# Kernel tuning notes

Measured on AMD Instinct MI355X. Metric: run time of the kernel, lower is better.

## Reference

```python
import jax, jax.numpy as jnp
import numpy as np

N, B, E, H = 131072, 4096, 512, 8
D = E // H

def setup_inputs() -> dict:
    key = jax.random.key(0)
    ks = jax.random.split(key, 20)
    def lin_w(k, fan_out, fan_in):
        return (jax.random.normal(k, (fan_out, fan_in), dtype=jnp.float32)
                * (1.0 / np.sqrt(fan_in)).astype(np.float32))
    node_features = jax.random.normal(ks[0], (N, E), dtype=jnp.float32)
    # segment ids sorted, guaranteed to cover every graph 0..B-1
    extra = jax.random.randint(ks[1], (N - B,), 0, B)
    batch = jnp.sort(jnp.concatenate([jnp.arange(B), extra])).astype(jnp.int32)
    scaffold_embedding = jax.random.normal(ks[2], (B, E), dtype=jnp.float32)
    return {
        'node_features': node_features,
        'scaffold_embedding': scaffold_embedding,
        'Wq': lin_w(ks[3], E, E), 'bq': jnp.zeros((E,), jnp.float32),
        'Wk': lin_w(ks[4], E, E), 'bk': jnp.zeros((E,), jnp.float32),
        'Wv': lin_w(ks[5], E, E), 'bv': jnp.zeros((E,), jnp.float32),
        'in_proj_w': lin_w(ks[6], 3 * E, E),
        'in_proj_b': jnp.zeros((3 * E,), jnp.float32),
        'mha_out_w': lin_w(ks[7], E, E), 'mha_out_b': jnp.zeros((E,), jnp.float32),
        'out_w': lin_w(ks[8], E, E), 'out_b': jnp.zeros((E,), jnp.float32),
        'ln_g': jnp.ones((E,), jnp.float32), 'ln_b': jnp.zeros((E,), jnp.float32),
        'batch': batch,
    }

def reference(node_features, scaffold_embedding, Wq, bq, Wk, bk, Wv, bv,
              in_proj_w, in_proj_b, mha_out_w, mha_out_b,
              out_w, out_b, ln_g, ln_b, batch):
    Bsz = scaffold_embedding.shape[0]
    # module's own q/k/v projections
    q = scaffold_embedding @ Wq.T + bq            # [B, E]
    k = node_features @ Wk.T + bk                 # [N, E]
    v = node_features @ Wv.T + bv                 # [N, E]
    # nn.MultiheadAttention internal in-projection
    Wiq, Wik, Wiv = jnp.split(in_proj_w, 3, axis=0)
    biq, bik, biv = jnp.split(in_proj_b, 3, axis=0)
    qq = (q @ Wiq.T + biq).reshape(Bsz, H, D)     # [B, H, D]
    kk = (k @ Wik.T + bik).reshape(-1, H, D)      # [N, H, D]
    vv = (v @ Wiv.T + biv).reshape(-1, H, D)      # [N, H, D]
    # per-node logit against its graph's single query (segment attention)
    scale = 1.0 / np.sqrt(D).astype(np.float32)
    logits = jnp.einsum('nhd,nhd->nh', kk, qq[batch]) * scale  # [N, H]
    m = jax.ops.segment_max(logits, batch, num_segments=B)     # [B, H]
    p = jnp.exp(logits - m[batch])
    Z = jax.ops.segment_sum(p, batch, num_segments=B)          # [B, H]
    w = p / Z[batch]                                           # [N, H]
    pooled = jax.ops.segment_sum(w[:, :, None] * vv, batch,
                                 num_segments=B).reshape(Bsz, E)
    # MHA out-projection, then module out_proj, dropout (eval=identity), LayerNorm
    out = pooled @ mha_out_w.T + mha_out_b
    out = out @ out_w.T + out_b
    mu = out.mean(axis=-1, keepdims=True)
    var = out.var(axis=-1, keepdims=True)
    return (out - mu) / jnp.sqrt(var + 1e-5) * ln_g + ln_b
```

## Files before the change

kernel.cpp:

```cpp
#include <hip/hip_runtime.h>
#include <hip/hip_bf16.h>
#include <cstdint>
#include <type_traits>

typedef __attribute__((ext_vector_type(8))) short short8v;
typedef __attribute__((ext_vector_type(8))) unsigned short ushort8v;
typedef __attribute__((ext_vector_type(4))) float f32x4;

__device__ __forceinline__ unsigned short f2bf(float f) {
    unsigned u = __builtin_bit_cast(unsigned, f);
    u = (u + 0x7fffu + ((u >> 16) & 1u)) >> 16;
    return (unsigned short)u;
}
__device__ __forceinline__ float bf2f(unsigned short s) {
    return __builtin_bit_cast(float, ((unsigned)s) << 16);
}
__device__ __forceinline__ unsigned cvtpk(float lo, float hi) {
    unsigned r;
    asm("v_cvt_pk_bf16_f32 %0, %1, %2" : "=v"(r) : "v"(lo), "v"(hi));
    return r;
}

template <typename TA, typename TW, bool C_BF16>
__device__ __forceinline__ void gemm_core(
    const TA* __restrict__ A, int lda,
    const TW* __restrict__ W, int ldw,
    void* __restrict__ Cp, int ldc,
    const float* __restrict__ bias, int K, size_t cbase,
    int bx, int by, unsigned short* As, unsigned short* Bs)
{
    const int tid  = threadIdx.x;
    const int lane = tid & 63;
    const int wave = tid >> 6;
    const int wr = wave >> 1, wc = wave & 1;
    const size_t row0 = (size_t)by * 128;
    const size_t col0 = (size_t)bx * 128;
    const int nk = K >> 6;

    f32x4 acc[4][4];
#pragma unroll
    for (int i = 0; i < 4; ++i)
#pragma unroll
        for (int j = 0; j < 4; ++j) acc[i][j] = f32x4{0.f, 0.f, 0.f, 0.f};

    float saf[4][8]; ushort8v sab[4];
    float swf[4][8]; ushort8v swb[4];

    auto load_tile = [&](int kt) {
#pragma unroll
        for (int it = 0; it < 4; ++it) {
            int g = tid + it * 256;
            int r = g >> 3, c8 = g & 7;
            if constexpr (std::is_same<TA, float>::value) {
                const float4* ap = reinterpret_cast<const float4*>(A + (row0 + r) * (size_t)lda + kt * 64 + c8 * 8);
                float4 a0 = ap[0], a1 = ap[1];
                saf[it][0] = a0.x; saf[it][1] = a0.y; saf[it][2] = a0.z; saf[it][3] = a0.w;
                saf[it][4] = a1.x; saf[it][5] = a1.y; saf[it][6] = a1.z; saf[it][7] = a1.w;
            } else {
                sab[it] = *reinterpret_cast<const ushort8v*>(A + (row0 + r) * (size_t)lda + kt * 64 + c8 * 8);
            }
            if constexpr (std::is_same<TW, float>::value) {
                const float4* wp = reinterpret_cast<const float4*>(W + (col0 + r) * (size_t)ldw + kt * 64 + c8 * 8);
                float4 w0 = wp[0], w1 = wp[1];
                swf[it][0] = w0.x; swf[it][1] = w0.y; swf[it][2] = w0.z; swf[it][3] = w0.w;
                swf[it][4] = w1.x; swf[it][5] = w1.y; swf[it][6] = w1.z; swf[it][7] = w1.w;
            } else {
                swb[it] = *reinterpret_cast<const ushort8v*>(W + (col0 + r) * (size_t)ldw + kt * 64 + c8 * 8);
            }
        }
    };
    auto write_tile = [&]() {
#pragma unroll
        for (int it = 0; it < 4; ++it) {
            int g = tid + it * 256;
            int r = g >> 3, c8 = g & 7;
            int idx = r * 64 + ((c8 ^ (r & 7)) << 3);
            if constexpr (std::is_same<TA, float>::value) {
                uint4 av;
                av.x = cvtpk(saf[it][0], saf[it][1]); av.y = cvtpk(saf[it][2], saf[it][3]);
                av.z = cvtpk(saf[it][4], saf[it][5]); av.w = cvtpk(saf[it][6], saf[it][7]);
                *reinterpret_cast<uint4*>(&As[idx]) = av;
            } else {
                *reinterpret_cast<ushort8v*>(&As[idx]) = sab[it];
            }
            if constexpr (std::is_same<TW, float>::value) {
                uint4 wv;
                wv.x = cvtpk(swf[it][0], swf[it][1]); wv.y = cvtpk(swf[it][2], swf[it][3]);
                wv.z = cvtpk(swf[it][4], swf[it][5]); wv.w = cvtpk(swf[it][6], swf[it][7]);
                *reinterpret_cast<uint4*>(&Bs[idx]) = wv;
            } else {
                *reinterpret_cast<ushort8v*>(&Bs[idx]) = swb[it];
            }
        }
    };

    load_tile(0);
    for (int kt = 0; kt < nk; ++kt) {
        __syncthreads();
        write_tile();
        __syncthreads();
        if (kt + 1 < nk) load_tile(kt + 1);
#pragma unroll
        for (int kk = 0; kk < 2; ++kk) {
            short8v af[4], bfv[4];
#pragma unroll
            for (int mi = 0; mi < 4; ++mi) {
                int r = wr * 64 + mi * 16 + (lane & 15);
                int slot = kk * 4 + (lane >> 4);
                af[mi] = *reinterpret_cast<const short8v*>(&As[r * 64 + ((slot ^ (r & 7)) << 3)]);
            }
#pragma unroll
            for (int ni = 0; ni < 4; ++ni) {
                int r = wc * 64 + ni * 16 + (lane & 15);
                int slot = kk * 4 + (lane >> 4);
                bfv[ni] = *reinterpret_cast<const short8v*>(&Bs[r * 64 + ((slot ^ (r & 7)) << 3)]);
            }
#pragma unroll
            for (int mi = 0; mi < 4; ++mi)
#pragma unroll
                for (int ni = 0; ni < 4; ++ni)
                    acc[mi][ni] = __builtin_amdgcn_mfma_f32_16x16x32_bf16(af[mi], bfv[ni], acc[mi][ni], 0, 0, 0);
        }
    }

#pragma unroll
    for (int ni = 0; ni < 4; ++ni) {
        size_t col = col0 + wc * 64 + ni * 16 + (lane & 15);
        float bv = bias ? bias[col] : 0.0f;
#pragma unroll
        for (int mi = 0; mi < 4; ++mi) {
#pragma unroll
            for (int q = 0; q < 4; ++q) {
                size_t row = row0 + wr * 64 + mi * 16 + ((lane >> 4) << 2) + q;
                float v = acc[mi][ni][q] + bv;
                if constexpr (C_BF16)
                    ((unsigned short*)Cp)[cbase + row * (size_t)ldc + col] = f2bf(v);
                else
                    ((float*)Cp)[cbase + row * (size_t)ldc + col] = v;
            }
        }
    }
}

template <typename TA, typename TW, bool C_BF16>
__global__ __launch_bounds__(256) void gemm_awt(
    const TA* __restrict__ A, int lda, const TW* __restrict__ W, int ldw,
    void* __restrict__ Cp, int ldc, const float* __restrict__ bias, int K,
    int az, int wz, size_t cz)
{
    __shared__ __attribute__((aligned(16))) unsigned short As[128 * 64];
    __shared__ __attribute__((aligned(16))) unsigned short Bs[128 * 64];
    gemm_core<TA, TW, C_BF16>(A + (size_t)blockIdx.z * az, lda,
                              W + (size_t)blockIdx.z * wz, ldw,
                              Cp, ldc, bias, K, (size_t)blockIdx.z * cz,
                              blockIdx.x, blockIdx.y, As, Bs);
}

struct WG4 { const float* A[4]; const float* W[4]; unsigned short* C[4]; };
__global__ __launch_bounds__(256) void gemm_w4(WG4 a)
{
    __shared__ __attribute__((aligned(16))) unsigned short As[128 * 64];
    __shared__ __attribute__((aligned(16))) unsigned short Bs[128 * 64];
    int z = blockIdx.z;
    gemm_core<float, float, true>(a.A[z], 512, a.W[z], 512, a.C[z], 512,
                                  nullptr, 512, 0, blockIdx.x, blockIdx.y, As, Bs);
}

__global__ void transpose4_512(const float* __restrict__ s0, float* __restrict__ d0,
                               const float* __restrict__ s1, float* __restrict__ d1,
                               const float* __restrict__ s2, float* __restrict__ d2,
                               const float* __restrict__ s3, float* __restrict__ d3)
{
    const float* src; float* dst;
    switch (blockIdx.z) {
        case 0: src = s0; dst = d0; break;
        case 1: src = s1; dst = d1; break;
        case 2: src = s2; dst = d2; break;
        default: src = s3; dst = d3; break;
    }
    __shared__ float t[32][33];
    int tx = threadIdx.x, ty = threadIdx.y;
    int bx = blockIdx.x * 32, by = blockIdx.y * 32;
#pragma unroll
    for (int j = 0; j < 4; ++j) t[ty + j * 8][tx] = src[(size_t)(by + ty + j * 8) * 512 + bx + tx];
    __syncthreads();
#pragma unroll
    for (int j = 0; j < 4; ++j) dst[(size_t)(bx + ty + j * 8) * 512 + by + tx] = t[tx][ty + j * 8];
}

struct BiasArgs { const float* W[3]; const float* vin[3]; const float* vadd[3]; float* out[3]; };
__global__ void bias_combine3(BiasArgs a)
{
    int which = blockIdx.y, e = blockIdx.x, lane = threadIdx.x;
    const float* W = a.W[which] + (size_t)e * 512 + lane * 8;
    const float* v = a.vin[which] + lane * 8;
    float s = 0.f;
#pragma unroll
    for (int j = 0; j < 8; ++j) s += W[j] * v[j];
#pragma unroll
    for (int st = 1; st < 64; st <<= 1) s += __shfl_xor(s, st, 64);
    if (lane == 0) a.out[which][e] = s + a.vadd[which][e];
}
__global__ void bias_combine_bf(const unsigned short* __restrict__ W, const float* __restrict__ vin,
                                const float* __restrict__ vadd, float* __restrict__ out)
{
    int e = blockIdx.x, lane = threadIdx.x;
    ushort8v wv = *reinterpret_cast<const ushort8v*>(W + (size_t)e * 512 + lane * 8);
    const float* v = vin + lane * 8;
    float s = 0.f;
#pragma unroll
    for (int j = 0; j < 8; ++j) s += bf2f(wv[j]) * v[j];
#pragma unroll
    for (int st = 1; st < 64; st <<= 1) s += __shfl_xor(s, st, 64);
    if (lane == 0) out[e] = s + vadd[e];
}

#define CHUNK 32
__global__ __launch_bounds__(256) void attn_pool(
    const float* __restrict__ X, const unsigned short* __restrict__ G,
    const int* __restrict__ batch, unsigned short* __restrict__ xw, int Nn)
{
    __shared__ __attribute__((aligned(16))) unsigned short Xs[CHUNK * 512];
    __shared__ __attribute__((aligned(16))) unsigned short Gs[8 * 512];
    __shared__ float lg[CHUNK * 8];
    __shared__ float red[256];
    __shared__ float mh[8], Zh[8], sch[8];

    const int b = blockIdx.x, t = threadIdx.x;
    const int lane = t & 63, wvx = t >> 6;

    int lo = 0, hi = Nn;
    while (lo < hi) { int mid = (lo + hi) >> 1; if (batch[mid] < b) lo = mid + 1; else hi = mid; }
    const int s = lo;
    hi = Nn;
    while (lo < hi) { int mid = (lo + hi) >> 1; if (batch[mid] < b + 1) lo = mid + 1; else hi = mid; }
    const int e = lo;

    if (t < 8) { mh[t] = -1e30f; Zh[t] = 0.f; }
    {
        const uint4* gp = reinterpret_cast<const uint4*>(G + (size_t)b * 4096);
        reinterpret_cast<uint4*>(Gs)[t] = gp[t];
        reinterpret_cast<uint4*>(Gs)[t + 256] = gp[t + 256];
    }

    float acc[16];
#pragma unroll
    for (int i = 0; i < 16; ++i) acc[i] = 0.f;

    for (int base = s; base < e; base += CHUNK) {
        const int cnt = min(CHUNK, e - base);
        __syncthreads();
#pragma unroll
        for (int i = 0; i < 8; ++i) {
            int u = t + 256 * i;
            int j = u >> 6;
            int col = (u & 63) * 8;
            uint4 w;
            if (j < cnt) {
                const float4* ap = reinterpret_cast<const float4*>(X + (size_t)(base + j) * 512 + col);
                float4 a0 = ap[0], a1 = ap[1];
                w.x = cvtpk(a0.x, a0.y); w.y = cvtpk(a0.z, a0.w);
                w.z = cvtpk(a1.x, a1.y); w.w = cvtpk(a1.z, a1.w);
            } else {
                w = uint4{0, 0, 0, 0};
            }
            *reinterpret_cast<uint4*>(&Xs[u * 8]) = w;
        }
        lg[t] = -1e30f;
        __syncthreads();
        for (int j = wvx; j < cnt; j += 4) {
            ushort8v xv = *reinterpret_cast<const ushort8v*>(&Xs[j * 512 + lane * 8]);
            float xf[8];
#pragma unroll
            for (int q = 0; q < 8; ++q) xf[q] = bf2f(xv[q]);
            float a8[8];
#pragma unroll
            for (int h = 0; h < 8; ++h) {
                ushort8v gv = *reinterpret_cast<const ushort8v*>(&Gs[h * 512 + lane * 8]);
                float sdot = 0.f;
#pragma unroll
                for (int q = 0; q < 8; ++q) sdot += xf[q] * bf2f(gv[q]);
                a8[h] = sdot;
            }
#pragma unroll
            for (int h = 0; h < 8; ++h)
#pragma unroll
                for (int st = 1; st < 64; st <<= 1) a8[h] += __shfl_xor(a8[h], st, 64);
            float ov = 0.f;
#pragma unroll
            for (int h = 0; h < 8; ++h) if (lane == h) ov = a8[h];
            if (lane < 8) lg[j * 8 + lane] = 0.125f * ov;
        }
        __syncthreads();
        red[t] = lg[t];
        __syncthreads();
        for (int st = 128; st >= 8; st >>= 1) { if (t < st) red[t] = fmaxf(red[t], red[t + st]); __syncthreads(); }
        if (t < 8) {
            float mnew = fmaxf(mh[t], red[t]);
            sch[t] = __expf(mh[t] - mnew);
            mh[t] = mnew;
        }
        __syncthreads();
        float pv = __expf(lg[t] - mh[t & 7]);
        lg[t] = pv;
        red[t] = pv;
        __syncthreads();
        for (int st = 128; st >= 8; st >>= 1) { if (t < st) red[t] += red[t + st]; __syncthreads(); }
        if (t < 8) Zh[t] = Zh[t] * sch[t] + red[t];
        float sc[8];
#pragma unroll
        for (int h = 0; h < 8; ++h) sc[h] = sch[h];
#pragma unroll
        for (int i = 0; i < 16; ++i) acc[i] *= sc[i >> 1];
        for (int j = 0; j < cnt; ++j) {
            float x0 = bf2f(Xs[j * 512 + t]);
            float x1 = bf2f(Xs[j * 512 + t + 256]);
#pragma unroll
            for (int h = 0; h < 8; ++h) {
                float pj = lg[j * 8 + h];
                acc[2 * h]     += pj * x0;
                acc[2 * h + 1] += pj * x1;
            }
        }
    }
    __syncthreads();
#pragma unroll
    for (int i = 0; i < 16; ++i) {
        float v = acc[i] / Zh[i >> 1];
        xw[(size_t)b * 4096 + t + 256 * i] = f2bf(v);
    }
}

__global__ __launch_bounds__(256) void ln_kernel(
    const float* __restrict__ X, const float* __restrict__ gam,
    const float* __restrict__ bet, float* __restrict__ out)
{
    int r = blockIdx.x, t = threadIdx.x;
    float v0 = X[(size_t)r * 512 + t], v1 = X[(size_t)r * 512 + t + 256];
    __shared__ float red[256];
    red[t] = v0 + v1; __syncthreads();
    for (int st = 128; st >= 1; st >>= 1) { if (t < st) red[t] += red[t + st]; __syncthreads(); }
    float mean = red[0] * (1.0f / 512.0f);
    __syncthreads();
    red[t] = v0 * v0 + v1 * v1; __syncthreads();
    for (int st = 128; st >= 1; st >>= 1) { if (t < st) red[t] += red[t + st]; __syncthreads(); }
    float var = red[0] * (1.0f / 512.0f) - mean * mean;
    float rstd = rsqrtf(var + 1e-5f);
    out[(size_t)r * 512 + t]       = (v0 - mean) * rstd * gam[t] + bet[t];
    out[(size_t)r * 512 + t + 256] = (v1 - mean) * rstd * gam[t + 256] + bet[t + 256];
}

extern "C" void kernel_launch(void* const* d_in, const int* in_sizes, int n_in,
                              void* d_out, int out_size, void* d_ws, size_t ws_size,
                              hipStream_t stream)
{
    const float* X   = (const float*)d_in[0];
    const float* SC  = (const float*)d_in[1];
    const float* Wq  = (const float*)d_in[2];
    const float* bq  = (const float*)d_in[3];
    const float* Wk  = (const float*)d_in[4];
    const float* bk  = (const float*)d_in[5];
    const float* Wv  = (const float*)d_in[6];
    const float* bv  = (const float*)d_in[7];
    const float* Wip = (const float*)d_in[8];
    const float* bip = (const float*)d_in[9];
    const float* Wmo = (const float*)d_in[10];
    const float* bmo = (const float*)d_in[11];
    const float* Wo  = (const float*)d_in[12];
    const float* bo  = (const float*)d_in[13];
    const float* lng = (const float*)d_in[14];
    const float* lnb = (const float*)d_in[15];
    const int*   batch = (const int*)d_in[16];

    const int Nn = in_sizes[0] / 512;
    const int Bz = in_sizes[1] / 512;

    const float* Wiq = Wip;
    const float* Wik = Wip + 512 * 512;
    const float* Wiv = Wip + 2 * 512 * 512;
    const float* biq = bip;
    const float* bik = bip + 512;
    const float* biv = bip + 1024;
    (void)bik;

    char* p = (char*)d_ws;
    auto alloc = [&](size_t bytes) -> char* {
        char* r = p; p += (bytes + 255) & ~(size_t)255; return r;
    };
    float* WkT  = (float*)alloc(512 * 512 * 4);
    float* WqT  = (float*)alloc(512 * 512 * 4);
    float* WvT  = (float*)alloc(512 * 512 * 4);
    float* WmoT = (float*)alloc(512 * 512 * 4);
    unsigned short* Wqq   = (unsigned short*)alloc(512 * 512 * 2);
    unsigned short* WkkT  = (unsigned short*)alloc(512 * 512 * 2);
    unsigned short* WvvT  = (unsigned short*)alloc(512 * 512 * 2);
    unsigned short* Woutc = (unsigned short*)alloc(512 * 512 * 2);
    unsigned short* Wbig  = (unsigned short*)alloc(512 * 4096 * 2);
    float* bqq   = (float*)alloc(512 * 4);
    float* bvv   = (float*)alloc(512 * 4);
    float* bou   = (float*)alloc(512 * 4);
    float* bias2 = (float*)alloc(512 * 4);
    float* QQ  = (float*)alloc((size_t)Bz * 512 * 4);
    unsigned short* G  = (unsigned short*)alloc((size_t)Bz * 8 * 512 * 2);
    unsigned short* xw = (unsigned short*)alloc((size_t)Bz * 4096 * 2);
    float* out1 = (float*)alloc((size_t)Bz * 512 * 4);

    transpose4_512<<<dim3(16, 16, 4), dim3(32, 8), 0, stream>>>(Wk, WkT, Wq, WqT, Wv, WvT, Wmo, WmoT);

    BiasArgs ba;
    ba.W[0] = Wiq; ba.vin[0] = bq;  ba.vadd[0] = biq; ba.out[0] = bqq;
    ba.W[1] = Wiv; ba.vin[1] = bv;  ba.vadd[1] = biv; ba.out[1] = bvv;
    ba.W[2] = Wo;  ba.vin[2] = bmo; ba.vadd[2] = bo;  ba.out[2] = bou;
    bias_combine3<<<dim3(512, 3), 64, 0, stream>>>(ba);

    WG4 wg;
    wg.A[0] = Wiq; wg.W[0] = WqT;  wg.C[0] = Wqq;
    wg.A[1] = WkT; wg.W[1] = Wik;  wg.C[1] = WkkT;
    wg.A[2] = WvT; wg.W[2] = Wiv;  wg.C[2] = WvvT;
    wg.A[3] = Wo;  wg.W[3] = WmoT; wg.C[3] = Woutc;
    gemm_w4<<<dim3(4, 4, 4), 256, 0, stream>>>(wg);

    bias_combine_bf<<<512, 64, 0, stream>>>(Woutc, bvv, bou, bias2);

    gemm_awt<unsigned short, unsigned short, true><<<dim3(4, 4, 8), 256, 0, stream>>>(
        Woutc, 512, WvvT, 512, Wbig, 4096, nullptr, 64, 64, 64, 512);

    gemm_awt<float, unsigned short, false><<<dim3(4, Bz / 128), 256, 0, stream>>>(
        SC, 512, Wqq, 512, QQ, 512, bqq, 512, 0, 0, 0);

    gemm_awt<float, unsigned short, true><<<dim3(4, Bz / 128, 8), 256, 0, stream>>>(
        QQ, 512, WkkT, 512, G, 4096, nullptr, 64, 64, 64, 512);

    attn_pool<<<Bz, 256, 0, stream>>>(X, G, batch, xw, Nn);

    gemm_awt<unsigned short, unsigned short, false><<<dim3(4, Bz / 128), 256, 0, stream>>>(
        xw, 4096, Wbig, 4096, out1, 512, bias2, 4096, 0, 0, 0);

    ln_kernel<<<Bz, 256, 0, stream>>>(out1, lng, lnb, (float*)d_out);
}
```

Baseline: 613.0 us.

## Rewrite segment attention pooling as per-head half-wave streaming kernel with split-K out GEMM

Replaces the block-level chunked attention pooling, which staged X through shared memory with many barriers and reductions, with a per-head half-wave kernel. Each half-wave streams node rows straight from global memory with a one-row prefetch, keeps an online softmax in registers and uses a lazy rescale that only triggers when the running max grows by more than 8. Segment bounds are now computed once by a separate kernel instead of a binary search in every block. The final 4096-deep GEMM is split along K into four partial outputs that reuse the G buffer, and the LayerNorm kernel sums them and adds the bias. The risks are serial per-row latency inside the streaming loop and extra partial-sum traffic.

```diff
diff --git a/kernel.cpp b/kernel.cpp
--- a/kernel.cpp
+++ b/kernel.cpp
@@ -215,128 +215,97 @@
     if (lane == 0) out[e] = s + vadd[e];
 }
 
-#define CHUNK 32
-__global__ __launch_bounds__(256) void attn_pool(
+__global__ void seg_bounds(const int* __restrict__ batch, int* __restrict__ segs, int Nn, int Bz)
+{
+    int n = blockIdx.x * 256 + threadIdx.x;
+    if (n >= Nn) return;
+    int b0 = batch[n];
+    int b1 = (n + 1 < Nn) ? batch[n + 1] : Bz;
+    for (int b = b0 + 1; b <= b1; ++b) segs[b] = n + 1;
+    if (n == 0) for (int b = 0; b <= b0; ++b) segs[b] = 0;
+}
+
+__global__ __launch_bounds__(256, 4) void attn_pool_wave(
     const float* __restrict__ X, const unsigned short* __restrict__ G,
-    const int* __restrict__ batch, unsigned short* __restrict__ xw, int Nn)
-{
-    __shared__ __attribute__((aligned(16))) unsigned short Xs[CHUNK * 512];
-    __shared__ __attribute__((aligned(16))) unsigned short Gs[8 * 512];
-    __shared__ float lg[CHUNK * 8];
-    __shared__ float red[256];
-    __shared__ float mh[8], Zh[8], sch[8];
-
-    const int b = blockIdx.x, t = threadIdx.x;
-    const int lane = t & 63, wvx = t >> 6;
-
-    int lo = 0, hi = Nn;
-    while (lo < hi) { int mid = (lo + hi) >> 1; if (batch[mid] < b) lo = mid + 1; else hi = mid; }
-    const int s = lo;
-    hi = Nn;
-    while (lo < hi) { int mid = (lo + hi) >> 1; if (batch[mid] < b + 1) lo = mid + 1; else hi = mid; }
-    const int e = lo;
-
-    if (t < 8) { mh[t] = -1e30f; Zh[t] = 0.f; }
+    const int* __restrict__ segs, unsigned short* __restrict__ xw)
+{
+    const int b    = blockIdx.x;
+    const int wid  = threadIdx.x >> 6;
+    const int lane = threadIdx.x & 63;
+    const int h    = wid * 2 + (lane >> 5);
+    const int kb   = lane & 31;
+    const int s = segs[b], e = segs[b + 1];
+
+    float g[16];
     {
-        const uint4* gp = reinterpret_cast<const uint4*>(G + (size_t)b * 4096);
-        reinterpret_cast<uint4*>(Gs)[t] = gp[t];
-        reinterpret_cast<uint4*>(Gs)[t + 256] = gp[t + 256];
+        const ushort8v* gp = reinterpret_cast<const ushort8v*>(G + ((size_t)b * 8 + h) * 512 + kb * 16);
+        ushort8v g0 = gp[0], g1 = gp[1];
+#pragma unroll
+        for (int q = 0; q < 8; ++q) { g[q] = bf2f(g0[q]); g[8 + q] = bf2f(g1[q]); }
     }
 
     float acc[16];
 #pragma unroll
     for (int i = 0; i < 16; ++i) acc[i] = 0.f;
-
-    for (int base = s; base < e; base += CHUNK) {
-        const int cnt = min(CHUNK, e - base);
-        __syncthreads();
-#pragma unroll
-        for (int i = 0; i < 8; ++i) {
-            int u = t + 256 * i;
-            int j = u >> 6;
-            int col = (u & 63) * 8;
-            uint4 w;
-            if (j < cnt) {
-                const float4* ap = reinterpret_cast<const float4*>(X + (size_t)(base + j) * 512 + col);
-                float4 a0 = ap[0], a1 = ap[1];
-                w.x = cvtpk(a0.x, a0.y); w.y = cvtpk(a0.z, a0.w);
-                w.z = cvtpk(a1.x, a1.y); w.w = cvtpk(a1.z, a1.w);
-            } else {
-                w = uint4{0, 0, 0, 0};
-            }
-            *reinterpret_cast<uint4*>(&Xs[u * 8]) = w;
+    float m = -1e30f, Z = 0.f;
+
+    const float4* xr = reinterpret_cast<const float4*>(X + (size_t)s * 512 + kb * 16);
+    float4 c0 = xr[0], c1 = xr[1], c2 = xr[2], c3 = xr[3];
+
+    for (int j = s; j < e; ++j) {
+        int jn = (j + 1 < e) ? j + 1 : j;
+        const float4* xn = reinterpret_cast<const float4*>(X + (size_t)jn * 512 + kb * 16);
+        float4 n0 = xn[0], n1 = xn[1], n2 = xn[2], n3 = xn[3];
+
+        float p;
+        p  = c0.x * g[0]  + c0.y * g[1]  + c0.z * g[2]  + c0.w * g[3];
+        p += c1.x * g[4]  + c1.y * g[5]  + c1.z * g[6]  + c1.w * g[7];
+        p += c2.x * g[8]  + c2.y * g[9]  + c2.z * g[10] + c2.w * g[11];
+        p += c3.x * g[12] + c3.y * g[13] + c3.z * g[14] + c3.w * g[15];
+#pragma unroll
+        for (int st = 1; st < 32; st <<= 1) p += __shfl_xor(p, st, 64);
+        p *= 0.125f;
+
+        if (p > m + 8.f) {
+            float sc = __expf(m - p);
+#pragma unroll
+            for (int i = 0; i < 16; ++i) acc[i] *= sc;
+            Z *= sc;
+            m = p;
         }
-        lg[t] = -1e30f;
-        __syncthreads();
-        for (int j = wvx; j < cnt; j += 4) {
-            ushort8v xv = *reinterpret_cast<const ushort8v*>(&Xs[j * 512 + lane * 8]);
-            float xf[8];
-#pragma unroll
-            for (int q = 0; q < 8; ++q) xf[q] = bf2f(xv[q]);
-            float a8[8];
-#pragma unroll
-            for (int h = 0; h < 8; ++h) {
-                ushort8v gv = *reinterpret_cast<const ushort8v*>(&Gs[h * 512 + lane * 8]);
-                float sdot = 0.f;
-#pragma unroll
-                for (int q = 0; q < 8; ++q) sdot += xf[q] * bf2f(gv[q]);
-                a8[h] = sdot;
-            }
-#pragma unroll
-            for (int h = 0; h < 8; ++h)
-#pragma unroll
-                for (int st = 1; st < 64; st <<= 1) a8[h] += __shfl_xor(a8[h], st, 64);
-            float ov = 0.f;
-#pragma unroll
-            for (int h = 0; h < 8; ++h) if (lane == h) ov = a8[h];
-            if (lane < 8) lg[j * 8 + lane] = 0.125f * ov;
-        }
-        __syncthreads();
-        red[t] = lg[t];
-        __syncthreads();
-        for (int st = 128; st >= 8; st >>= 1) { if (t < st) red[t] = fmaxf(red[t], red[t + st]); __syncthreads(); }
-        if (t < 8) {
-            float mnew = fmaxf(mh[t], red[t]);
-            sch[t] = __expf(mh[t] - mnew);
-            mh[t] = mnew;
-        }
-        __syncthreads();
-        float pv = __expf(lg[t] - mh[t & 7]);
-        lg[t] = pv;
-        red[t] = pv;
-        __syncthreads();
-        for (int st = 128; st >= 8; st >>= 1) { if (t < st) red[t] += red[t + st]; __syncthreads(); }
-        if (t < 8) Zh[t] = Zh[t] * sch[t] + red[t];
-        float sc[8];
-#pragma unroll
-        for (int h = 0; h < 8; ++h) sc[h] = sch[h];
-#pragma unroll
-        for (int i = 0; i < 16; ++i) acc[i] *= sc[i >> 1];
-        for (int j = 0; j < cnt; ++j) {
-            float x0 = bf2f(Xs[j * 512 + t]);
-            float x1 = bf2f(Xs[j * 512 + t + 256]);
-#pragma unroll
-            for (int h = 0; h < 8; ++h) {
-                float pj = lg[j * 8 + h];
-                acc[2 * h]     += pj * x0;
-                acc[2 * h + 1] += pj * x1;
-            }
-        }
-    }
-    __syncthreads();
-#pragma unroll
-    for (int i = 0; i < 16; ++i) {
-        float v = acc[i] / Zh[i >> 1];
-        xw[(size_t)b * 4096 + t + 256 * i] = f2bf(v);
-    }
-}
-
-__global__ __launch_bounds__(256) void ln_kernel(
-    const float* __restrict__ X, const float* __restrict__ gam,
-    const float* __restrict__ bet, float* __restrict__ out)
+        float w = __expf(p - m);
+        Z += w;
+        acc[0]  += w * c0.x; acc[1]  += w * c0.y; acc[2]  += w * c0.z; acc[3]  += w * c0.w;
+        acc[4]  += w * c1.x; acc[5]  += w * c1.y; acc[6]  += w * c1.z; acc[7]  += w * c1.w;
+        acc[8]  += w * c2.x; acc[9]  += w * c2.y; acc[10] += w * c2.z; acc[11] += w * c2.w;
+        acc[12] += w * c3.x; acc[13] += w * c3.y; acc[14] += w * c3.z; acc[15] += w * c3.w;
+
+        c0 = n0; c1 = n1; c2 = n2; c3 = n3;
+    }
+
+    float iz = 1.0f / Z;
+    uint4 o0, o1;
+    o0.x = cvtpk(acc[0] * iz, acc[1] * iz);   o0.y = cvtpk(acc[2] * iz, acc[3] * iz);
+    o0.z = cvtpk(acc[4] * iz, acc[5] * iz);   o0.w = cvtpk(acc[6] * iz, acc[7] * iz);
+    o1.x = cvtpk(acc[8] * iz, acc[9] * iz);   o1.y = cvtpk(acc[10] * iz, acc[11] * iz);
+    o1.z = cvtpk(acc[12] * iz, acc[13] * iz); o1.w = cvtpk(acc[14] * iz, acc[15] * iz);
+    unsigned short* op = xw + (size_t)b * 4096 + h * 512 + kb * 16;
+    reinterpret_cast<uint4*>(op)[0] = o0;
+    reinterpret_cast<uint4*>(op)[1] = o1;
+}
+
+__global__ __launch_bounds__(256) void ln4_kernel(
+    const float* __restrict__ parts, int Bz, const float* __restrict__ bias2,
+    const float* __restrict__ gam, const float* __restrict__ bet, float* __restrict__ out)
 {
     int r = blockIdx.x, t = threadIdx.x;
-    float v0 = X[(size_t)r * 512 + t], v1 = X[(size_t)r * 512 + t + 256];
+    size_t M = (size_t)Bz * 512;
+    float v0 = bias2[t], v1 = bias2[t + 256];
+#pragma unroll
+    for (int z = 0; z < 4; ++z) {
+        v0 += parts[z * M + (size_t)r * 512 + t];
+        v1 += parts[z * M + (size_t)r * 512 + t + 256];
+    }
     __shared__ float red[256];
     red[t] = v0 + v1; __syncthreads();
     for (int st = 128; st >= 1; st >>= 1) { if (t < st) red[t] += red[t + st]; __syncthreads(); }
@@ -379,9 +348,7 @@
     const float* Wik = Wip + 512 * 512;
     const float* Wiv = Wip + 2 * 512 * 512;
     const float* biq = bip;
-    const float* bik = bip + 512;
     const float* biv = bip + 1024;
-    (void)bik;
 
     char* p = (char*)d_ws;
     auto alloc = [&](size_t bytes) -> char* {
@@ -403,7 +370,8 @@
     float* QQ  = (float*)alloc((size_t)Bz * 512 * 4);
     unsigned short* G  = (unsigned short*)alloc((size_t)Bz * 8 * 512 * 2);
     unsigned short* xw = (unsigned short*)alloc((size_t)Bz * 4096 * 2);
-    float* out1 = (float*)alloc((size_t)Bz * 512 * 4);
+    int* segs = (int*)alloc((size_t)(Bz + 1) * 4);
+    float* parts = (float*)G;
 
     transpose4_512<<<dim3(16, 16, 4), dim3(32, 8), 0, stream>>>(Wk, WkT, Wq, WqT, Wv, WvT, Wmo, WmoT);
 
@@ -412,6 +380,8 @@
     ba.W[1] = Wiv; ba.vin[1] = bv;  ba.vadd[1] = biv; ba.out[1] = bvv;
     ba.W[2] = Wo;  ba.vin[2] = bmo; ba.vadd[2] = bo;  ba.out[2] = bou;
     bias_combine3<<<dim3(512, 3), 64, 0, stream>>>(ba);
+
+    seg_bounds<<<(Nn + 255) / 256, 256, 0, stream>>>(batch, segs, Nn, Bz);
 
     WG4 wg;
     wg.A[0] = Wiq; wg.W[0] = WqT;  wg.C[0] = Wqq;
@@ -431,10 +401,10 @@
     gemm_awt<float, unsigned short, true><<<dim3(4, Bz / 128, 8), 256, 0, stream>>>(
         QQ, 512, WkkT, 512, G, 4096, nullptr, 64, 64, 64, 512);
 
-    attn_pool<<<Bz, 256, 0, stream>>>(X, G, batch, xw, Nn);
-
-    gemm_awt<unsigned short, unsigned short, false><<<dim3(4, Bz / 128), 256, 0, stream>>>(
-        xw, 4096, Wbig, 4096, out1, 512, bias2, 4096, 0, 0, 0);
-
-    ln_kernel<<<Bz, 256, 0, stream>>>(out1, lng, lnb, (float*)d_out);
-}
+    attn_pool_wave<<<Bz, 256, 0, stream>>>(X, G, segs, xw);
+
+    gemm_awt<unsigned short, unsigned short, false><<<dim3(4, Bz / 128, 4), 256, 0, stream>>>(
+        xw, 4096, Wbig, 4096, parts, 512, nullptr, 1024, 1024, 1024, (size_t)Bz * 512);
+
+    ln4_kernel<<<Bz, 256, 0, stream>>>(parts, Bz, bias2, lng, lnb, (float*)d_out);
+}
```

Measured after the change: 564.4 us. 7.9% less time.
